# Performance work log

Hardware: AMD Instinct MI355X
Metric: run time of the kernel (lower is better)

Reference implementation:

```python
import jax, jax.numpy as jnp
import numpy as np


def _conv1x1_relu(x, w, b):
    # x: [B,C,T,H,W], w: [O,C], b: [O] -> 1x1x1 conv + ReLU
    y = jnp.einsum('oc,bcthw->bothw', w, x) + b[None, :, None, None, None]
    return jax.nn.relu(y)


def _maxpool3d_2(x):
    # MaxPool3d(kernel=2, stride=2, padding=0) over T,H,W
    return jax.lax.reduce_window(
        x, -jnp.inf, jax.lax.max,
        window_dimensions=(1, 1, 2, 2, 2),
        window_strides=(1, 1, 2, 2, 2),
        padding='VALID')


def setup_inputs() -> dict:
    key = jax.random.key(0)
    ks = jax.random.split(key, 10)
    B, C, T, H, W = 4, 128, 16, 32, 32
    C1, C2 = 4, 2
    d1, d2 = C // C1, C // C2  # 32, 64
    s = 0.05
    return {
        'x':  jax.random.normal(ks[0], (B, C, T, H, W), dtype=jnp.float32),
        'wf': jax.random.normal(ks[1], (d1, C), dtype=jnp.float32) * s,
        'bf': jnp.zeros((d1,), dtype=jnp.float32),
        'wg': jax.random.normal(ks[2], (d1, C), dtype=jnp.float32) * s,
        'bg': jnp.zeros((d1,), dtype=jnp.float32),
        'wh': jax.random.normal(ks[3], (d2, C), dtype=jnp.float32) * s,
        'bh': jnp.zeros((d2,), dtype=jnp.float32),
        'wo': jax.random.normal(ks[4], (C, d2), dtype=jnp.float32) * s,
        'bo': jnp.zeros((C,), dtype=jnp.float32),
        'gamma': jnp.asarray([0.5], dtype=jnp.float32),
    }


def reference(x, wf, bf, wg, bg, wh, bh, wo, bo, gamma):
    B, C, T, H, W = x.shape
    N = T * H * W
    theta = _conv1x1_relu(x, wf, bf).reshape(B, wf.shape[0], N)          # [B,d1,N]
    phi = _maxpool3d_2(_conv1x1_relu(x, wg, bg)).reshape(B, wg.shape[0], N // 8)  # [B,d1,M]
    g = _maxpool3d_2(_conv1x1_relu(x, wh, bh)).reshape(B, wh.shape[0], N // 8)    # [B,d2,M]
    # attn = softmax(theta^T @ phi) over keys (no 1/sqrt(d) scaling, as in source)
    scores = jnp.einsum('bcn,bcm->bnm', theta, phi)                      # [B,N,M]
    attn = jax.nn.softmax(scores, axis=-1)
    attn_g = jnp.einsum('bcm,bnm->bcn', g, attn).reshape(B, wh.shape[0], T, H, W)
    out = x + gamma[0] * _conv1x1_relu(attn_g, wo, bo)
    return out
```

## Files before the change

kernel.cpp:

```cpp
#include <hip/hip_runtime.h>
#include <hip/hip_bf16.h>

#define NB 4
#define NC 128
#define NN 16384
#define NM 2048

typedef __attribute__((ext_vector_type(8))) short bf16x8;
typedef __attribute__((ext_vector_type(4))) float f32x4;
typedef __attribute__((ext_vector_type(4))) unsigned short u16x4;
typedef __attribute__((ext_vector_type(2))) unsigned int u32x2;

#define MFMA16(a,b,c) __builtin_amdgcn_mfma_f32_16x16x32_bf16((a),(b),(c),0,0,0)

__device__ __forceinline__ unsigned short f2bf(float f){
  unsigned int u = __float_as_uint(f);
  u += 0x7fffu + ((u >> 16) & 1u);
  return (unsigned short)(u >> 16);
}
__device__ __forceinline__ float bf2f(unsigned short h){
  return __uint_as_float(((unsigned int)h) << 16);
}
__device__ __forceinline__ unsigned int packbf2(float lo, float hi){
  return (__float_as_uint(hi) & 0xffff0000u) | (__float_as_uint(lo) >> 16);
}

__global__ void k0_prep(const float* __restrict__ wf, const float* __restrict__ wg,
                        const float* __restrict__ wh, const float* __restrict__ bfp,
                        const float* __restrict__ bgp, const float* __restrict__ bhp,
                        const float* __restrict__ wo,
                        unsigned short* __restrict__ Wcat, unsigned short* __restrict__ wob,
                        float* __restrict__ bcat){
  int i = blockIdx.x * 256 + threadIdx.x;
  if (i < 16384){
    int o = i >> 7, c = i & 127;
    float v = (o < 32) ? wf[o*128 + c] : (o < 64) ? wg[(o-32)*128 + c] : wh[(o-64)*128 + c];
    Wcat[i] = f2bf(v);
  } else if (i < 24576){
    wob[i - 16384] = f2bf(wo[i - 16384]);
  } else if (i < 24704){
    int k = i - 24576;
    bcat[k] = (k < 32) ? bfp[k] : (k < 64) ? bgp[k-32] : bhp[k-64];
  }
}

__global__ __launch_bounds__(256, 4) void k2_conv(
    const float* __restrict__ x, const unsigned short* __restrict__ Wcat,
    const float* __restrict__ bcat,
    unsigned short* __restrict__ thetaT, unsigned short* __restrict__ Ywh){
  __shared__ __align__(16) unsigned short xtile[64][132];
  __shared__ unsigned short Ytmp[96][33];
  int blk = blockIdx.x;
  int b = blk >> 8, nblk = blk & 255;
  int n0 = nblk * 64;
  int tid = threadIdx.x;

  {
    int c = tid >> 1, half = tid & 1;
    const float* xr = x + ((size_t)(b*128 + c)) * NN + n0 + half*32;
    #pragma unroll
    for (int j = 0; j < 8; ++j){
      float4 v = *(const float4*)(xr + j*4);
      int nl = half*32 + j*4;
      xtile[nl+0][c] = f2bf(v.x);
      xtile[nl+1][c] = f2bf(v.y);
      xtile[nl+2][c] = f2bf(v.z);
      xtile[nl+3][c] = f2bf(v.w);
    }
  }
  __syncthreads();

  int lane = tid & 63, w = tid >> 6;
  int ln = lane & 15, gq = lane >> 4;
  int n = n0 + w*16 + ln;
  bf16x8 xf[4];
  #pragma unroll
  for (int kf = 0; kf < 4; ++kf)
    xf[kf] = *(const bf16x8*)(&xtile[w*16 + ln][kf*32 + gq*8]);

  #pragma unroll
  for (int ot = 0; ot < 8; ++ot){
    f32x4 acc = {0.f,0.f,0.f,0.f};
    #pragma unroll
    for (int kf = 0; kf < 4; ++kf){
      bf16x8 wfr = *(const bf16x8*)(Wcat + (ot*16 + ln)*128 + kf*32 + gq*8);
      acc = MFMA16(wfr, xf[kf], acc);
    }
    float y[4];
    #pragma unroll
    for (int i = 0; i < 4; ++i){
      int o = ot*16 + gq*4 + i;
      float v = acc[i] + bcat[o];
      y[i] = v > 0.f ? v : 0.f;
    }
    if (ot < 2){
      u16x4 pk;
      #pragma unroll
      for (int i = 0; i < 4; ++i) pk[i] = f2bf(y[i]);
      *(u16x4*)(thetaT + ((size_t)b*NN + n)*32 + ot*16 + gq*4) = pk;
    } else {
      #pragma unroll
      for (int i = 0; i < 4; ++i){
        float ym = fmaxf(y[i], __shfl_xor(y[i], 1));
        if ((ln & 1) == 0){
          int r = ot*16 + gq*4 + i - 32;
          Ytmp[r][(w*16 + ln) >> 1] = f2bf(ym);
        }
      }
    }
  }
  __syncthreads();

  int tt = n0 >> 10;
  int h2 = nblk & 15;
  #pragma unroll
  for (int q = 0; q < 6; ++q){
    int idx = q*256 + tid;
    int r = idx >> 4, j = idx & 15;
    unsigned short a = Ytmp[r][j], bsh = Ytmp[r][j+16];
    unsigned short v = a > bsh ? a : bsh;
    Ywh[(((size_t)(b*96 + r))*16 + tt)*256 + h2*16 + j] = v;
  }
}

__global__ void k3_pool(const unsigned short* __restrict__ Ywh,
                        unsigned short* __restrict__ phiT, unsigned short* __restrict__ g_){
  __shared__ unsigned short trans[64][36];
  int blk = blockIdx.x;
  int t = threadIdx.x;
  if (blk < 128){
    int b = blk >> 5, mseg = blk & 31;
    int m0 = mseg * 64;
    int u = m0 >> 8, p0 = m0 & 255;
    int c = t >> 3, mj = t & 7;
    const unsigned short* r0 = Ywh + (((size_t)(b*96 + c))*16 + 2*u)*256 + p0 + mj*8;
    const unsigned short* r1 = r0 + 256;
    #pragma unroll
    for (int k = 0; k < 8; ++k){
      unsigned short a = r0[k], bsh = r1[k];
      trans[mj*8 + k][c] = a > bsh ? a : bsh;
    }
    __syncthreads();
    int ml = t >> 2, cg = t & 3;
    u16x4 o0, o1;
    #pragma unroll
    for (int k = 0; k < 4; ++k){ o0[k] = trans[ml][cg*8 + k]; o1[k] = trans[ml][cg*8 + 4 + k]; }
    *(u16x4*)(phiT + ((size_t)b*NM + m0 + ml)*32 + cg*8)     = o0;
    *(u16x4*)(phiT + ((size_t)b*NM + m0 + ml)*32 + cg*8 + 4) = o1;
  } else {
    int blk2 = blk - 128;
    int b = blk2 >> 6, c2 = blk2 & 63;
    int u = t >> 5, p = (t & 31) * 8;
    const unsigned short* r0 = Ywh + (((size_t)(b*96 + 32 + c2))*16 + 2*u)*256 + p;
    const unsigned short* r1 = r0 + 256;
    u16x4 o0, o1;
    #pragma unroll
    for (int k = 0; k < 4; ++k){
      unsigned short a0 = r0[k],   b0 = r1[k];
      unsigned short a1 = r0[4+k], b1 = r1[4+k];
      o0[k] = a0 > b0 ? a0 : b0;
      o1[k] = a1 > b1 ? a1 : b1;
    }
    *(u16x4*)(g_ + ((size_t)(b*64 + c2))*NM + t*8)     = o0;
    *(u16x4*)(g_ + ((size_t)(b*64 + c2))*NM + t*8 + 4) = o1;
  }
}

__global__ __launch_bounds__(256, 4) void k4_attn(
    const unsigned short* __restrict__ thetaT, const unsigned short* __restrict__ phiT,
    const unsigned short* __restrict__ g_, unsigned short* __restrict__ pacc,
    float* __restrict__ lsumA){
  __shared__ __align__(16) unsigned short phi_lds[2][32][40];
  __shared__ __align__(16) unsigned short g_lds[2][64][40];
  __shared__ __align__(16) unsigned short P_lds[4][16][40];

  int bx = blockIdx.x;
  int b = bx >> 8, qb = (bx >> 1) & 127, kh = bx & 1;
  int tid = threadIdx.x;
  int lane = tid & 63, wv = tid >> 6;
  int ln = lane & 15, gq = lane >> 4;
  int nq = qb*128 + wv*32;
  int ch0 = kh * 32;

  const unsigned short* thb = thetaT + (size_t)b*NN*32;
  const unsigned short* phb = phiT   + (size_t)b*NM*32;
  const unsigned short* gb  = g_     + (size_t)b*64*NM;

  bf16x8 thf0 = *(const bf16x8*)(thb + (size_t)(nq + ln)*32 + gq*8);
  bf16x8 thf1 = *(const bf16x8*)(thb + (size_t)(nq + 16 + ln)*32 + gq*8);

  f32x4 acc[2][4];
  #pragma unroll
  for (int q = 0; q < 2; ++q)
    #pragma unroll
    for (int c2t = 0; c2t < 4; ++c2t) acc[q][c2t] = (f32x4){0.f,0.f,0.f,0.f};
  float lsum0 = 0.f, lsum1 = 0.f;

  int gr = tid >> 2, gp = tid & 3;
  const unsigned short* sgp_g = gb + (size_t)gr*NM + ch0*32 + gp*8;
  unsigned short* slg0 = &g_lds[0][gr][gp*8];
  unsigned short* slg1 = &g_lds[1][gr][gp*8];
  bool hasphi = tid < 128;
  int pr = (tid >> 2) & 31, pp = tid & 3;
  const unsigned short* sgp_p = phb + ((size_t)(ch0*32 + pr))*32 + pp*8;
  unsigned short* slp0 = &phi_lds[0][pr][pp*8];
  unsigned short* slp1 = &phi_lds[1][pr][pp*8];

  { bf16x8 srg = *(const bf16x8*)(sgp_g); *(bf16x8*)slg0 = srg; }
  if (hasphi){ bf16x8 srp = *(const bf16x8*)(sgp_p); *(bf16x8*)slp0 = srp; }
  __syncthreads();

  bf16x8 srg_n = {}, srp_n = {};
  for (int lc = 0; lc < 32; ++lc){
    int cur = lc & 1;
    if (lc + 1 < 32){
      srg_n = *(const bf16x8*)(sgp_g + (size_t)(lc+1)*32);
      if (hasphi) srp_n = *(const bf16x8*)(sgp_p + (size_t)(lc+1)*1024);
    }
    bf16x8 pf0 = *(const bf16x8*)(&phi_lds[cur][ln][gq*8]);
    bf16x8 pf1 = *(const bf16x8*)(&phi_lds[cur][16+ln][gq*8]);
    bf16x8 gf0 = *(const bf16x8*)(&g_lds[cur][ln][gq*8]);
    bf16x8 gf1 = *(const bf16x8*)(&g_lds[cur][16+ln][gq*8]);
    bf16x8 gf2 = *(const bf16x8*)(&g_lds[cur][32+ln][gq*8]);
    bf16x8 gf3 = *(const bf16x8*)(&g_lds[cur][48+ln][gq*8]);
    f32x4 z = {0.f,0.f,0.f,0.f};

    {
      f32x4 s0 = MFMA16(pf0, thf0, z);
      f32x4 s1 = MFMA16(pf1, thf0, z);
      float p0[4], p1[4];
      #pragma unroll
      for (int i = 0; i < 4; ++i){ p0[i] = __expf(s0[i]); p1[i] = __expf(s1[i]); }
      lsum0 += ((p0[0]+p0[1]) + (p0[2]+p0[3])) + ((p1[0]+p1[1]) + (p1[2]+p1[3]));
      u32x2 w0 = { packbf2(p0[0],p0[1]), packbf2(p0[2],p0[3]) };
      u32x2 w1 = { packbf2(p1[0],p1[1]), packbf2(p1[2],p1[3]) };
      *(u32x2*)(&P_lds[wv][ln][gq*4])      = w0;
      *(u32x2*)(&P_lds[wv][ln][16+gq*4])   = w1;
      bf16x8 paf = *(const bf16x8*)(&P_lds[wv][ln][gq*8]);
      acc[0][0] = MFMA16(paf, gf0, acc[0][0]);
      acc[0][1] = MFMA16(paf, gf1, acc[0][1]);
      acc[0][2] = MFMA16(paf, gf2, acc[0][2]);
      acc[0][3] = MFMA16(paf, gf3, acc[0][3]);
    }
    {
      f32x4 s0 = MFMA16(pf0, thf1, z);
      f32x4 s1 = MFMA16(pf1, thf1, z);
      float p0[4], p1[4];
      #pragma unroll
      for (int i = 0; i < 4; ++i){ p0[i] = __expf(s0[i]); p1[i] = __expf(s1[i]); }
      lsum1 += ((p0[0]+p0[1]) + (p0[2]+p0[3])) + ((p1[0]+p1[1]) + (p1[2]+p1[3]));
      u32x2 w0 = { packbf2(p0[0],p0[1]), packbf2(p0[2],p0[3]) };
      u32x2 w1 = { packbf2(p1[0],p1[1]), packbf2(p1[2],p1[3]) };
      *(u32x2*)(&P_lds[wv][ln][gq*4])      = w0;
      *(u32x2*)(&P_lds[wv][ln][16+gq*4])   = w1;
      bf16x8 paf = *(const bf16x8*)(&P_lds[wv][ln][gq*8]);
      acc[1][0] = MFMA16(paf, gf0, acc[1][0]);
      acc[1][1] = MFMA16(paf, gf1, acc[1][1]);
      acc[1][2] = MFMA16(paf, gf2, acc[1][2]);
      acc[1][3] = MFMA16(paf, gf3, acc[1][3]);
    }
    if (lc + 1 < 32){
      *(bf16x8*)(((lc+1)&1) ? slg1 : slg0) = srg_n;
      if (hasphi) *(bf16x8*)(((lc+1)&1) ? slp1 : slp0) = srp_n;
    }
    __syncthreads();
  }

  lsum0 += __shfl_xor(lsum0, 16); lsum0 += __shfl_xor(lsum0, 32);
  lsum1 += __shfl_xor(lsum1, 16); lsum1 += __shfl_xor(lsum1, 32);

  unsigned short* pb = pacc + ((size_t)(kh*NB + b))*NN*64;
  #pragma unroll
  for (int i = 0; i < 4; ++i){
    int r0 = nq + gq*4 + i, r1 = nq + 16 + gq*4 + i;
    #pragma unroll
    for (int c2t = 0; c2t < 4; ++c2t){
      pb[(size_t)r0*64 + c2t*16 + ln] = f2bf(acc[0][c2t][i]);
      pb[(size_t)r1*64 + c2t*16 + ln] = f2bf(acc[1][c2t][i]);
    }
  }
  size_t lbase = ((size_t)(kh*NB + b))*NN;
  if (gq == 0)      lsumA[lbase + nq + ln]      = lsum0;
  else if (gq == 1) lsumA[lbase + nq + 16 + ln] = lsum1;
}

__device__ __forceinline__ bf16x8 combine8(bf16x8 a, bf16x8 b, float inv){
  bf16x8 r;
  #pragma unroll
  for (int k = 0; k < 8; ++k){
    float f = (bf2f((unsigned short)a[k]) + bf2f((unsigned short)b[k])) * inv;
    r[k] = (short)f2bf(f);
  }
  return r;
}

__global__ __launch_bounds__(256, 4) void k5_out(
    const float* __restrict__ x, const unsigned short* __restrict__ pacc,
    const float* __restrict__ lsumA,
    const unsigned short* __restrict__ wob, const float* __restrict__ bo,
    const float* __restrict__ gamma, float* __restrict__ out){
  int blk = blockIdx.x;
  int b = blk >> 8, nblk = blk & 255;
  int tid = threadIdx.x;
  int lane = tid & 63, w = tid >> 6;
  int ln = lane & 15, gq = lane >> 4;
  int n = nblk*64 + w*16 + ln;

  const unsigned short* p0 = pacc + ((size_t)b*NN + n)*64;
  const unsigned short* p1 = pacc + ((size_t)(NB + b)*NN + n)*64;
  float l = lsumA[(size_t)b*NN + n] + lsumA[(size_t)(NB + b)*NN + n];
  float inv = 1.0f / l;
  bf16x8 a0lo = *(const bf16x8*)(p0 + gq*8);
  bf16x8 a1lo = *(const bf16x8*)(p1 + gq*8);
  bf16x8 a0hi = *(const bf16x8*)(p0 + 32 + gq*8);
  bf16x8 a1hi = *(const bf16x8*)(p1 + 32 + gq*8);
  bf16x8 bfr0 = combine8(a0lo, a1lo, inv);
  bf16x8 bfr1 = combine8(a0hi, a1hi, inv);

  float gam = gamma[0];
  #pragma unroll
  for (int ot = 0; ot < 8; ++ot){
    f32x4 acc = {0.f,0.f,0.f,0.f};
    bf16x8 a0 = *(const bf16x8*)(wob + (ot*16 + ln)*64 + gq*8);
    bf16x8 a1 = *(const bf16x8*)(wob + (ot*16 + ln)*64 + 32 + gq*8);
    acc = MFMA16(a0, bfr0, acc);
    acc = MFMA16(a1, bfr1, acc);
    #pragma unroll
    for (int i = 0; i < 4; ++i){
      int o = ot*16 + gq*4 + i;
      size_t idx = ((size_t)b*128 + o)*NN + n;
      float v = acc[i] + bo[o];
      v = v > 0.f ? v : 0.f;
      out[idx] = x[idx] + gam * v;
    }
  }
}

extern "C" void kernel_launch(void* const* d_in, const int* in_sizes, int n_in,
                              void* d_out, int out_size, void* d_ws, size_t ws_size,
                              hipStream_t stream){
  const float* x   = (const float*)d_in[0];
  const float* wf  = (const float*)d_in[1];
  const float* bfp = (const float*)d_in[2];
  const float* wg  = (const float*)d_in[3];
  const float* bgp = (const float*)d_in[4];
  const float* wh  = (const float*)d_in[5];
  const float* bhp = (const float*)d_in[6];
  const float* wo  = (const float*)d_in[7];
  const float* bo  = (const float*)d_in[8];
  const float* gam = (const float*)d_in[9];
  float* out = (float*)d_out;
  char* ws = (char*)d_ws;

  const size_t OFF_WCAT = 0;
  const size_t OFF_WO   = 32768;
  const size_t OFF_BCAT = 49152;
  const size_t OFF_TH   = 65536;
  const size_t OFF_YWH  = OFF_TH  + (size_t)NB*NN*32*2;
  const size_t OFF_PHI  = OFF_YWH + (size_t)NB*96*16*256*2;
  const size_t OFF_G    = OFF_PHI + (size_t)NB*NM*32*2;
  const size_t OFF_PACC = OFF_G   + (size_t)NB*64*NM*2;
  const size_t OFF_LSUM = OFF_PACC+ (size_t)2*NB*NN*64*2;

  unsigned short* Wcat    = (unsigned short*)(ws + OFF_WCAT);
  unsigned short* wob     = (unsigned short*)(ws + OFF_WO);
  float*          bcat    = (float*)(ws + OFF_BCAT);
  unsigned short* thetaT  = (unsigned short*)(ws + OFF_TH);
  unsigned short* Ywh     = (unsigned short*)(ws + OFF_YWH);
  unsigned short* phiT    = (unsigned short*)(ws + OFF_PHI);
  unsigned short* g_      = (unsigned short*)(ws + OFF_G);
  unsigned short* pacc    = (unsigned short*)(ws + OFF_PACC);
  float*          lsumA   = (float*)(ws + OFF_LSUM);

  k0_prep<<<97, 256, 0, stream>>>(wf, wg, wh, bfp, bgp, bhp, wo, Wcat, wob, bcat);
  k2_conv<<<1024, 256, 0, stream>>>(x, Wcat, bcat, thetaT, Ywh);
  k3_pool<<<384, 256, 0, stream>>>(Ywh, phiT, g_);
  k4_attn<<<1024, 256, 0, stream>>>(thetaT, phiT, g_, pacc, lsumA);
  k5_out<<<1024, 256, 0, stream>>>(x, pacc, lsumA, wob, bo, gam, out);
}
```

Measured before the change: 170.0 us.

## Stage conv input, theta output and final residual through LDS for coalesced access

k2_conv now loads x with each thread reading 8 channels × 4 positions and writes 16-byte packed bf16 rows into LDS instead of scalar transposed stores. Its theta output is staged in shared memory and written out as full 16-byte rows. k5_out buffers gamma*relu(conv) in a 34 KB LDS tile, then does the x read and out write as contiguous float4 rows, replacing scattered 4-byte accesses. This adds LDS footprint and a barrier, which may lower occupancy in k5.

Result: slower. 176.7 us (+4.0%).

```diff
diff --git a/kernel.cpp b/kernel.cpp
--- a/kernel.cpp
+++ b/kernel.cpp
@@ -10,15 +10,16 @@
 typedef __attribute__((ext_vector_type(4))) float f32x4;
 typedef __attribute__((ext_vector_type(4))) unsigned short u16x4;
 typedef __attribute__((ext_vector_type(2))) unsigned int u32x2;
+typedef unsigned short us;
 
 #define MFMA16(a,b,c) __builtin_amdgcn_mfma_f32_16x16x32_bf16((a),(b),(c),0,0,0)
 
-__device__ __forceinline__ unsigned short f2bf(float f){
+__device__ __forceinline__ us f2bf(float f){
   unsigned int u = __float_as_uint(f);
   u += 0x7fffu + ((u >> 16) & 1u);
-  return (unsigned short)(u >> 16);
-}
-__device__ __forceinline__ float bf2f(unsigned short h){
+  return (us)(u >> 16);
+}
+__device__ __forceinline__ float bf2f(us h){
   return __uint_as_float(((unsigned int)h) << 16);
 }
 __device__ __forceinline__ unsigned int packbf2(float lo, float hi){
@@ -29,7 +30,7 @@
                         const float* __restrict__ wh, const float* __restrict__ bfp,
                         const float* __restrict__ bgp, const float* __restrict__ bhp,
                         const float* __restrict__ wo,
-                        unsigned short* __restrict__ Wcat, unsigned short* __restrict__ wob,
+                        us* __restrict__ Wcat, us* __restrict__ wob,
                         float* __restrict__ bcat){
   int i = blockIdx.x * 256 + threadIdx.x;
   if (i < 16384){
@@ -45,38 +46,42 @@
 }
 
 __global__ __launch_bounds__(256, 4) void k2_conv(
-    const float* __restrict__ x, const unsigned short* __restrict__ Wcat,
+    const float* __restrict__ x, const us* __restrict__ Wcat,
     const float* __restrict__ bcat,
-    unsigned short* __restrict__ thetaT, unsigned short* __restrict__ Ywh){
-  __shared__ __align__(16) unsigned short xtile[64][132];
-  __shared__ unsigned short Ytmp[96][33];
+    us* __restrict__ thetaT, us* __restrict__ Ywh){
+  __shared__ __align__(16) us xtile[64*136];
+  __shared__ __align__(16) us theta_sh[64*40];
+  __shared__ us Ytmp[96*33];
   int blk = blockIdx.x;
   int b = blk >> 8, nblk = blk & 255;
   int n0 = nblk * 64;
   int tid = threadIdx.x;
 
   {
-    int c = tid >> 1, half = tid & 1;
-    const float* xr = x + ((size_t)(b*128 + c)) * NN + n0 + half*32;
+    int nbase = (tid & 15) * 4;
+    int c0 = (tid >> 4) * 8;
+    float va[8][4];
     #pragma unroll
     for (int j = 0; j < 8; ++j){
-      float4 v = *(const float4*)(xr + j*4);
-      int nl = half*32 + j*4;
-      xtile[nl+0][c] = f2bf(v.x);
-      xtile[nl+1][c] = f2bf(v.y);
-      xtile[nl+2][c] = f2bf(v.z);
-      xtile[nl+3][c] = f2bf(v.w);
+      float4 v = *(const float4*)(x + ((size_t)(b*128 + c0 + j)) * NN + n0 + nbase);
+      va[j][0]=v.x; va[j][1]=v.y; va[j][2]=v.z; va[j][3]=v.w;
+    }
+    #pragma unroll
+    for (int nn = 0; nn < 4; ++nn){
+      bf16x8 r;
+      #pragma unroll
+      for (int j = 0; j < 8; ++j) r[j] = (short)f2bf(va[j][nn]);
+      *(bf16x8*)&xtile[(nbase+nn)*136 + c0] = r;
     }
   }
   __syncthreads();
 
   int lane = tid & 63, w = tid >> 6;
   int ln = lane & 15, gq = lane >> 4;
-  int n = n0 + w*16 + ln;
   bf16x8 xf[4];
   #pragma unroll
   for (int kf = 0; kf < 4; ++kf)
-    xf[kf] = *(const bf16x8*)(&xtile[w*16 + ln][kf*32 + gq*8]);
+    xf[kf] = *(const bf16x8*)&xtile[(w*16+ln)*136 + kf*32 + gq*8];
 
   #pragma unroll
   for (int ot = 0; ot < 8; ++ot){
@@ -97,35 +102,40 @@
       u16x4 pk;
       #pragma unroll
       for (int i = 0; i < 4; ++i) pk[i] = f2bf(y[i]);
-      *(u16x4*)(thetaT + ((size_t)b*NN + n)*32 + ot*16 + gq*4) = pk;
+      *(u16x4*)&theta_sh[(w*16+ln)*40 + ot*16 + gq*4] = pk;
     } else {
       #pragma unroll
       for (int i = 0; i < 4; ++i){
         float ym = fmaxf(y[i], __shfl_xor(y[i], 1));
         if ((ln & 1) == 0){
           int r = ot*16 + gq*4 + i - 32;
-          Ytmp[r][(w*16 + ln) >> 1] = f2bf(ym);
+          Ytmp[r*33 + ((w*16 + ln) >> 1)] = f2bf(ym);
         }
       }
     }
   }
   __syncthreads();
 
+  {
+    int row = tid >> 2, coff = (tid & 3) * 8;
+    bf16x8 tv = *(const bf16x8*)&theta_sh[row*40 + coff];
+    *(bf16x8*)(thetaT + ((size_t)b*NN + n0 + row)*32 + coff) = tv;
+  }
   int tt = n0 >> 10;
   int h2 = nblk & 15;
   #pragma unroll
   for (int q = 0; q < 6; ++q){
     int idx = q*256 + tid;
     int r = idx >> 4, j = idx & 15;
-    unsigned short a = Ytmp[r][j], bsh = Ytmp[r][j+16];
-    unsigned short v = a > bsh ? a : bsh;
+    us a = Ytmp[r*33 + j], bsh = Ytmp[r*33 + j + 16];
+    us v = a > bsh ? a : bsh;
     Ywh[(((size_t)(b*96 + r))*16 + tt)*256 + h2*16 + j] = v;
   }
 }
 
-__global__ void k3_pool(const unsigned short* __restrict__ Ywh,
-                        unsigned short* __restrict__ phiT, unsigned short* __restrict__ g_){
-  __shared__ unsigned short trans[64][36];
+__global__ void k3_pool(const us* __restrict__ Ywh,
+                        us* __restrict__ phiT, us* __restrict__ g_){
+  __shared__ us trans[64][36];
   int blk = blockIdx.x;
   int t = threadIdx.x;
   if (blk < 128){
@@ -133,11 +143,11 @@
     int m0 = mseg * 64;
     int u = m0 >> 8, p0 = m0 & 255;
     int c = t >> 3, mj = t & 7;
-    const unsigned short* r0 = Ywh + (((size_t)(b*96 + c))*16 + 2*u)*256 + p0 + mj*8;
-    const unsigned short* r1 = r0 + 256;
+    const us* r0 = Ywh + (((size_t)(b*96 + c))*16 + 2*u)*256 + p0 + mj*8;
+    const us* r1 = r0 + 256;
     #pragma unroll
     for (int k = 0; k < 8; ++k){
-      unsigned short a = r0[k], bsh = r1[k];
+      us a = r0[k], bsh = r1[k];
       trans[mj*8 + k][c] = a > bsh ? a : bsh;
     }
     __syncthreads();
@@ -151,13 +161,13 @@
     int blk2 = blk - 128;
     int b = blk2 >> 6, c2 = blk2 & 63;
     int u = t >> 5, p = (t & 31) * 8;
-    const unsigned short* r0 = Ywh + (((size_t)(b*96 + 32 + c2))*16 + 2*u)*256 + p;
-    const unsigned short* r1 = r0 + 256;
+    const us* r0 = Ywh + (((size_t)(b*96 + 32 + c2))*16 + 2*u)*256 + p;
+    const us* r1 = r0 + 256;
     u16x4 o0, o1;
     #pragma unroll
     for (int k = 0; k < 4; ++k){
-      unsigned short a0 = r0[k],   b0 = r1[k];
-      unsigned short a1 = r0[4+k], b1 = r1[4+k];
+      us a0 = r0[k],   b0 = r1[k];
+      us a1 = r0[4+k], b1 = r1[4+k];
       o0[k] = a0 > b0 ? a0 : b0;
       o1[k] = a1 > b1 ? a1 : b1;
     }
@@ -167,12 +177,12 @@
 }
 
 __global__ __launch_bounds__(256, 4) void k4_attn(
-    const unsigned short* __restrict__ thetaT, const unsigned short* __restrict__ phiT,
-    const unsigned short* __restrict__ g_, unsigned short* __restrict__ pacc,
+    const us* __restrict__ thetaT, const us* __restrict__ phiT,
+    const us* __restrict__ g_, us* __restrict__ pacc,
     float* __restrict__ lsumA){
-  __shared__ __align__(16) unsigned short phi_lds[2][32][40];
-  __shared__ __align__(16) unsigned short g_lds[2][64][40];
-  __shared__ __align__(16) unsigned short P_lds[4][16][40];
+  __shared__ __align__(16) us phi_lds[2][32][40];
+  __shared__ __align__(16) us g_lds[2][64][40];
+  __shared__ __align__(16) us P_lds[4][16][40];
 
   int bx = blockIdx.x;
   int b = bx >> 8, qb = (bx >> 1) & 127, kh = bx & 1;
@@ -182,9 +192,9 @@
   int nq = qb*128 + wv*32;
   int ch0 = kh * 32;
 
-  const unsigned short* thb = thetaT + (size_t)b*NN*32;
-  const unsigned short* phb = phiT   + (size_t)b*NM*32;
-  const unsigned short* gb  = g_     + (size_t)b*64*NM;
+  const us* thb = thetaT + (size_t)b*NN*32;
+  const us* phb = phiT   + (size_t)b*NM*32;
+  const us* gb  = g_     + (size_t)b*64*NM;
 
   bf16x8 thf0 = *(const bf16x8*)(thb + (size_t)(nq + ln)*32 + gq*8);
   bf16x8 thf1 = *(const bf16x8*)(thb + (size_t)(nq + 16 + ln)*32 + gq*8);
@@ -197,14 +207,14 @@
   float lsum0 = 0.f, lsum1 = 0.f;
 
   int gr = tid >> 2, gp = tid & 3;
-  const unsigned short* sgp_g = gb + (size_t)gr*NM + ch0*32 + gp*8;
-  unsigned short* slg0 = &g_lds[0][gr][gp*8];
-  unsigned short* slg1 = &g_lds[1][gr][gp*8];
+  const us* sgp_g = gb + (size_t)gr*NM + ch0*32 + gp*8;
+  us* slg0 = &g_lds[0][gr][gp*8];
+  us* slg1 = &g_lds[1][gr][gp*8];
   bool hasphi = tid < 128;
   int pr = (tid >> 2) & 31, pp = tid & 3;
-  const unsigned short* sgp_p = phb + ((size_t)(ch0*32 + pr))*32 + pp*8;
-  unsigned short* slp0 = &phi_lds[0][pr][pp*8];
-  unsigned short* slp1 = &phi_lds[1][pr][pp*8];
+  const us* sgp_p = phb + ((size_t)(ch0*32 + pr))*32 + pp*8;
+  us* slp0 = &phi_lds[0][pr][pp*8];
+  us* slp1 = &phi_lds[1][pr][pp*8];
 
   { bf16x8 srg = *(const bf16x8*)(sgp_g); *(bf16x8*)slg0 = srg; }
   if (hasphi){ bf16x8 srp = *(const bf16x8*)(sgp_p); *(bf16x8*)slp0 = srp; }
@@ -269,7 +279,7 @@
   lsum0 += __shfl_xor(lsum0, 16); lsum0 += __shfl_xor(lsum0, 32);
   lsum1 += __shfl_xor(lsum1, 16); lsum1 += __shfl_xor(lsum1, 32);
 
-  unsigned short* pb = pacc + ((size_t)(kh*NB + b))*NN*64;
+  us* pb = pacc + ((size_t)(kh*NB + b))*NN*64;
   #pragma unroll
   for (int i = 0; i < 4; ++i){
     int r0 = nq + gq*4 + i, r1 = nq + 16 + gq*4 + i;
@@ -288,26 +298,29 @@
   bf16x8 r;
   #pragma unroll
   for (int k = 0; k < 8; ++k){
-    float f = (bf2f((unsigned short)a[k]) + bf2f((unsigned short)b[k])) * inv;
+    float f = (bf2f((us)a[k]) + bf2f((us)b[k])) * inv;
     r[k] = (short)f2bf(f);
   }
   return r;
 }
 
 __global__ __launch_bounds__(256, 4) void k5_out(
-    const float* __restrict__ x, const unsigned short* __restrict__ pacc,
+    const float* __restrict__ x, const us* __restrict__ pacc,
     const float* __restrict__ lsumA,
-    const unsigned short* __restrict__ wob, const float* __restrict__ bo,
+    const us* __restrict__ wob, const float* __restrict__ bo,
     const float* __restrict__ gamma, float* __restrict__ out){
+  __shared__ __align__(16) float vt[128*68];
   int blk = blockIdx.x;
   int b = blk >> 8, nblk = blk & 255;
+  int n0 = nblk * 64;
   int tid = threadIdx.x;
   int lane = tid & 63, w = tid >> 6;
   int ln = lane & 15, gq = lane >> 4;
-  int n = nblk*64 + w*16 + ln;
-
-  const unsigned short* p0 = pacc + ((size_t)b*NN + n)*64;
-  const unsigned short* p1 = pacc + ((size_t)(NB + b)*NN + n)*64;
+  int n = n0 + w*16 + ln;
+  int nl = w*16 + ln;
+
+  const us* p0 = pacc + ((size_t)b*NN + n)*64;
+  const us* p1 = pacc + ((size_t)(NB + b)*NN + n)*64;
   float l = lsumA[(size_t)b*NN + n] + lsumA[(size_t)(NB + b)*NN + n];
   float inv = 1.0f / l;
   bf16x8 a0lo = *(const bf16x8*)(p0 + gq*8);
@@ -328,11 +341,23 @@
     #pragma unroll
     for (int i = 0; i < 4; ++i){
       int o = ot*16 + gq*4 + i;
-      size_t idx = ((size_t)b*128 + o)*NN + n;
       float v = acc[i] + bo[o];
       v = v > 0.f ? v : 0.f;
-      out[idx] = x[idx] + gam * v;
-    }
+      vt[o*68 + nl] = gam * v;
+    }
+  }
+  __syncthreads();
+
+  int o = tid >> 1, half = tid & 1;
+  const float* xr = x + ((size_t)b*128 + o)*NN + n0 + half*32;
+  float* outr = out + ((size_t)b*128 + o)*NN + n0 + half*32;
+  const float* vr = &vt[o*68 + half*32];
+  #pragma unroll
+  for (int k = 0; k < 8; ++k){
+    float4 xv = *(const float4*)(xr + k*4);
+    float4 dv = *(const float4*)(vr + k*4);
+    float4 ov = { xv.x + dv.x, xv.y + dv.y, xv.z + dv.z, xv.w + dv.w };
+    *(float4*)(outr + k*4) = ov;
   }
 }
 
@@ -362,15 +387,15 @@
   const size_t OFF_PACC = OFF_G   + (size_t)NB*64*NM*2;
   const size_t OFF_LSUM = OFF_PACC+ (size_t)2*NB*NN*64*2;
 
-  unsigned short* Wcat    = (unsigned short*)(ws + OFF_WCAT);
-  unsigned short* wob     = (unsigned short*)(ws + OFF_WO);
-  float*          bcat    = (float*)(ws + OFF_BCAT);
-  unsigned short* thetaT  = (unsigned short*)(ws + OFF_TH);
-  unsigned short* Ywh     = (unsigned short*)(ws + OFF_YWH);
-  unsigned short* phiT    = (unsigned short*)(ws + OFF_PHI);
-  unsigned short* g_      = (unsigned short*)(ws + OFF_G);
-  unsigned short* pacc    = (unsigned short*)(ws + OFF_PACC);
-  float*          lsumA   = (float*)(ws + OFF_LSUM);
+  us*    Wcat    = (us*)(ws + OFF_WCAT);
+  us*    wob     = (us*)(ws + OFF_WO);
+  float* bcat    = (float*)(ws + OFF_BCAT);
+  us*    thetaT  = (us*)(ws + OFF_TH);
+  us*    Ywh     = (us*)(ws + OFF_YWH);
+  us*    phiT    = (us*)(ws + OFF_PHI);
+  us*    g_      = (us*)(ws + OFF_G);
+  us*    pacc    = (us*)(ws + OFF_PACC);
+  float* lsumA   = (float*)(ws + OFF_LSUM);
 
   k0_prep<<<97, 256, 0, stream>>>(wf, wg, wh, bfp, bgp, bhp, wo, Wcat, wob, bcat);
   k2_conv<<<1024, 256, 0, stream>>>(x, Wcat, bcat, thetaT, Ywh);
```
